# Optimization experiments

Measured on AMD Instinct MI355X. Metric: run time of the kernel, lower is better.

## Reference

```python
import jax, jax.numpy as jnp
import numpy as np

NUM_EXPERTS = 8
HIDDEN = 2048
INTER = 1408
N_TOKENS = 8192


def setup_inputs() -> dict:
    key = jax.random.key(0)
    k1, k2, k3, k4, k5 = jax.random.split(key, 5)
    tokens = jax.random.normal(k1, (N_TOKENS, HIDDEN), dtype=jnp.float32)
    local_ids = jax.random.randint(k2, (N_TOKENS,), 0, NUM_EXPERTS)
    weights = jax.random.uniform(k3, (N_TOKENS,), dtype=jnp.float32)
    # kaiming_uniform-ish init scale
    bound1 = 1.0 / np.sqrt(HIDDEN)
    bound2 = 1.0 / np.sqrt(INTER)
    gate_up_proj = jax.random.uniform(k4, (NUM_EXPERTS, 2 * INTER, HIDDEN), dtype=jnp.float32, minval=-bound1, maxval=bound1)
    down_proj = jax.random.uniform(k5, (NUM_EXPERTS, HIDDEN, INTER), dtype=jnp.float32, minval=-bound2, maxval=bound2)
    return {"tokens": tokens, "local_ids": local_ids, "weights": weights,
            "gate_up_proj": gate_up_proj, "down_proj": down_proj}


def reference(tokens, local_ids, weights, gate_up_proj, down_proj):
    # tokens: [N, D]; local_ids: [N]; weights: [N]
    # gate_up_proj: [E, 2I, D]; down_proj: [E, D, I]
    E = gate_up_proj.shape[0]
    out = jnp.zeros_like(tokens)
    for e in range(E):  # fixed small expert loop; masked dense GEMMs
        fc1 = tokens @ gate_up_proj[e].T              # [N, 2I]
        gate, up = jnp.split(fc1, 2, axis=-1)         # SwiGLU convention: first half is gate
        h = jax.nn.silu(gate) * up                    # fused SiLU*up
        h = h * weights[:, None]                      # routing weight before down_proj
        o = h @ down_proj[e].T                        # [N, D]
        out = out + jnp.where((local_ids == e)[:, None], o, 0.0)
    return out
```

## Files before the change

kernel.cpp:

```cpp
#include <hip/hip_runtime.h>
#include <stdint.h>

#define E_    8
#define D_    2048
#define I_    1408
#define TWOI_ 2816
#define N_    8192
#define BM    128
#define MAXTILES 72
#define MPAD  9216
#define MAXST 40
#define NCT1  11

typedef __bf16 bf16x8 __attribute__((ext_vector_type(8)));
typedef float  floatx4 __attribute__((ext_vector_type(4)));

#define M_CNT   0
#define M_CUR   8
#define M_PB    16
#define M_NT    24
#define M_RTE   32
#define M_RTR   104
#define M_RTV   176
#define M_NST   248
#define M_STE   256
#define M_STR   296
#define M_STV   336

#define OFF_PERM  4096ULL
#define OFF_WPAD  40960ULL
#define OFF_APAD  81920ULL
#define OFF_HPAD  37830656ULL
#define OFF_GU    63782912ULL
#define OFF_DN    156057600ULL
#define WS_NEED   202194944ULL

__device__ inline void gload16(const void* g, void* lds) {
  __builtin_amdgcn_global_load_lds(
      (__attribute__((address_space(1))) void*)g,
      (__attribute__((address_space(3))) void*)lds, 16, 0, 0);
}

__device__ inline unsigned short f2bf(float f) {
  unsigned int u = __builtin_bit_cast(unsigned int, f);
  u += 0x7fffu + ((u >> 16) & 1u);
  return (unsigned short)(u >> 16);
}

__global__ void k_hist(const int* __restrict__ ids, int* meta) {
  int i = blockIdx.x * 256 + threadIdx.x;
  int e = ids[i];
  int lane = threadIdx.x & 63;
  for (int ex = 0; ex < E_; ++ex) {
    unsigned long long m = __ballot(e == ex);
    if (lane == 0 && m) atomicAdd(&meta[M_CNT + ex], __popcll(m));
  }
}

__global__ void k_meta(int* meta) {
  if (threadIdx.x != 0) return;
  int padr = 0, tiles = 0;
  for (int e = 0; e < E_; ++e) {
    meta[M_PB + e] = padr;
    int c = meta[M_CNT + e];
    int nt = (c + BM - 1) / BM;
    for (int t = 0; t < nt; ++t) {
      meta[M_RTE + tiles] = e;
      meta[M_RTR + tiles] = padr + t * BM;
      int v = c - t * BM; if (v > BM) v = BM;
      meta[M_RTV + tiles] = v;
      tiles++;
    }
    padr += nt * BM;
  }
  meta[M_NT] = tiles;
  int nst = 0;
  for (int e = 0; e < E_; ++e) {
    int c = meta[M_CNT + e];
    int pb = meta[M_PB + e];
    for (int off = 0; off < c; off += 256) {
      meta[M_STE + nst] = e;
      meta[M_STR + nst] = pb + off;
      int v = c - off; if (v > 256) v = 256;
      meta[M_STV + nst] = v;
      nst++;
    }
  }
  meta[M_NST] = nst;
}

__global__ void k_scatter(const int* __restrict__ ids, const float* __restrict__ w,
                          int* meta, int* perm, float* wpad) {
  int i = blockIdx.x * 256 + threadIdx.x;
  int e = ids[i];
  float wv = w[i];
  int lane = threadIdx.x & 63;
  for (int ex = 0; ex < E_; ++ex) {
    unsigned long long m = __ballot(e == ex);
    if (!m) continue;
    int base = 0;
    if (lane == 0) base = atomicAdd(&meta[M_CUR + ex], __popcll(m));
    base = __shfl(base, 0);
    if (e == ex) {
      int r = meta[M_PB + ex] + base + __popcll(m & ((1ULL << lane) - 1ULL));
      perm[r] = i;
      wpad[r] = wv;
    }
  }
}

__global__ void k_gather(const float* __restrict__ tokens, const int* __restrict__ perm,
                         unsigned short* __restrict__ apad) {
  int r = blockIdx.x;
  int t = perm[r];
  if (t < 0) return;
  const float4* src = (const float4*)(tokens + (size_t)t * D_);
  uint4* dst = (uint4*)(apad + (size_t)r * D_);
  int i = threadIdx.x;
  float4 a = src[i * 2], b = src[i * 2 + 1];
  union { unsigned short s[8]; uint4 v; } pk;
  pk.s[0] = f2bf(a.x); pk.s[1] = f2bf(a.y); pk.s[2] = f2bf(a.z); pk.s[3] = f2bf(a.w);
  pk.s[4] = f2bf(b.x); pk.s[5] = f2bf(b.y); pk.s[6] = f2bf(b.z); pk.s[7] = f2bf(b.w);
  dst[i] = pk.v;
}

__global__ void k_cvt(const float* __restrict__ src, unsigned short* __restrict__ dst, int n8) {
  int i = blockIdx.x * 256 + threadIdx.x;
  if (i >= n8) return;
  const float4* s4 = (const float4*)src;
  float4 a = s4[i * 2], b = s4[i * 2 + 1];
  union { unsigned short s[8]; uint4 v; } pk;
  pk.s[0] = f2bf(a.x); pk.s[1] = f2bf(a.y); pk.s[2] = f2bf(a.z); pk.s[3] = f2bf(a.w);
  pk.s[4] = f2bf(b.x); pk.s[5] = f2bf(b.y); pk.s[6] = f2bf(b.z); pk.s[7] = f2bf(b.w);
  ((uint4*)dst)[i] = pk.v;
}


#define RD_A(h, s)                                                            \
  {                                                                           \
    const char* baseA_ = (const char*)&Abuf[s][h][0];                         \
    _Pragma("unroll") for (int mf = 0; mf < 4; ++mf) {                        \
      af[mf][0] = *(const bf16x8*)(baseA_ + rbA + mf * 2048 + swz0);          \
      af[mf][1] = *(const bf16x8*)(baseA_ + rbA + mf * 2048 + swz1);          \
    }                                                                         \
  }

#define RD_B(h, s)                                                            \
  {                                                                           \
    const char* baseB_ = (const char*)&Bbuf[s][h][0];                         \
    _Pragma("unroll") for (int nf = 0; nf < 2; ++nf) {                        \
      bq[nf][0] = *(const bf16x8*)(baseB_ + cbB + nf * 2048 + swz0);          \
      bq[nf][1] = *(const bf16x8*)(baseB_ + cbB + nf * 2048 + swz1);          \
    }                                                                         \
  }

#define MFMA_PH(qi)                                                           \
  __builtin_amdgcn_s_setprio(1);                                              \
  _Pragma("unroll") for (int mf = 0; mf < 4; ++mf) {                          \
    _Pragma("unroll") for (int nf = 0; nf < 2; ++nf) {                        \
      acc[qi][mf][nf] = __builtin_amdgcn_mfma_f32_16x16x32_bf16(              \
          af[mf][0], bq[nf][0], acc[qi][mf][nf], 0, 0, 0);                    \
      acc[qi][mf][nf] = __builtin_amdgcn_mfma_f32_16x16x32_bf16(              \
          af[mf][1], bq[nf][1], acc[qi][mf][nf], 0, 0, 0);                    \
    }                                                                         \
  }                                                                           \
  __builtin_amdgcn_s_setprio(0);

#define PH_MID()                                                              \
  __builtin_amdgcn_sched_barrier(0);                                          \
  __builtin_amdgcn_s_barrier();                                               \
  asm volatile("s_waitcnt lgkmcnt(0)" ::: "memory");                          \
  __builtin_amdgcn_sched_barrier(0);

#define PH_END()    __builtin_amdgcn_s_barrier();
#define PH_END_V6() asm volatile("s_waitcnt vmcnt(6)" ::: "memory"); \
                    __builtin_amdgcn_s_barrier();
#define PH_END_V8() asm volatile("s_waitcnt vmcnt(8)" ::: "memory"); \
                    __builtin_amdgcn_s_barrier();

#define STAGE(P, BUF, s, h)                                                   \
  gload16(P, &BUF[s][h][ldst]);                                               \
  gload16(P + 64 * D_, &BUF[s][h][4096 + ldst]);                              \
  P += 64;

__global__ __launch_bounds__(512, 2) void k_gemm1(
    const unsigned short* __restrict__ apad,
    const unsigned short* __restrict__ gub,
    const float* __restrict__ wpad,
    const int* __restrict__ meta,
    unsigned short* __restrict__ hpad) {
  int nst = meta[M_NST];
  int active = nst * NCT1;
  int bid = blockIdx.x;
  if (bid >= active) return;
  int x = bid & 7, idx = bid >> 3;
  int q = active >> 3, r = active & 7;
  int wgid = (x < r ? x * (q + 1) : r * (q + 1) + (x - r) * q) + idx;
  int st = wgid / NCT1;
  int ct = wgid - st * NCT1;
  int e = meta[M_STE + st], row0 = meta[M_STR + st], nv = meta[M_STV + st];

  __shared__ __attribute__((aligned(16))) __bf16 Abuf[2][2][128 * 64];
  __shared__ __attribute__((aligned(16))) __bf16 Bbuf[2][2][128 * 64];

  int tid = threadIdx.x;
  int lane = tid & 63;
  int wave = __builtin_amdgcn_readfirstlane(tid >> 6);
  int wm = wave >> 2, wn = wave & 3;
  int l16 = lane & 15, qd = lane >> 4;

  int r0 = tid >> 3;
  int jl8 = (((tid >> 3) ^ tid) & 7) * 8;
  const __bf16* pa0 = (const __bf16*)apad + (size_t)(row0 + r0) * D_ + jl8;
  const __bf16* pa1 = pa0 + (size_t)128 * D_;
  const __bf16* pb0 = (const __bf16*)gub +
      ((size_t)e * TWOI_ + (size_t)ct * 128 + r0) * D_ + jl8;
  const __bf16* pb1 = pb0 + (size_t)I_ * D_;
  int ldst = wave * 512;

  int swz0 = ((qd ^ (l16 & 7)) & 7) * 16;
  int swz1 = (((4 + qd) ^ (l16 & 7)) & 7) * 16;
  int rbA = (wm * 64 + l16) * 128;
  int cbB = (wn * 32 + l16) * 128;

  floatx4 zero = {0.f, 0.f, 0.f, 0.f};
  floatx4 acc[4][4][2];
#pragma unroll
  for (int a = 0; a < 4; ++a)
#pragma unroll
    for (int b = 0; b < 4; ++b)
#pragma unroll
      for (int c = 0; c < 2; ++c) acc[a][b][c] = zero;

  STAGE(pa0, Abuf, 0, 0)
  STAGE(pb0, Bbuf, 0, 0)
  STAGE(pa1, Abuf, 0, 1)
  STAGE(pb1, Bbuf, 0, 1)
  STAGE(pa0, Abuf, 1, 0)
  STAGE(pb0, Bbuf, 1, 0)
  asm volatile("s_waitcnt vmcnt(8)" ::: "memory");
  __builtin_amdgcn_s_barrier();

  bf16x8 af[4][2], bq[2][2];
  for (int t = 0; t < 32; t += 2) {
#pragma unroll
    for (int u = 0; u < 2; ++u) {
      int tl = t + u;
      RD_A(0, u)
      RD_B(0, u)
      if (tl + 1 < 32) { STAGE(pa1, Abuf, u ^ 1, 1) }
      PH_MID()
      MFMA_PH(0)
      PH_END_V6()
      RD_B(1, u)
      if (tl + 1 < 32) { STAGE(pb1, Bbuf, u ^ 1, 1) }
      PH_MID()
      MFMA_PH(1)
      PH_END()
      RD_A(1, u)
      RD_B(0, u)
      if (tl + 2 < 32) { STAGE(pa0, Abuf, u, 0) }
      PH_MID()
      MFMA_PH(2)
      PH_END()
      RD_B(1, u)
      if (tl + 2 < 32) { STAGE(pb0, Bbuf, u, 0) }
      PH_MID()
      MFMA_PH(3)
      PH_END_V8()
    }
  }

#pragma unroll
  for (int mi2 = 0; mi2 < 2; ++mi2)
#pragma unroll
    for (int mf = 0; mf < 4; ++mf)
#pragma unroll
      for (int reg = 0; reg < 4; ++reg) {
        int lr = mi2 * 128 + wm * 64 + mf * 16 + qd * 4 + reg;
        if (lr < nv) {
          float wgt = wpad[row0 + lr];
          unsigned short* hrow = hpad + (size_t)(row0 + lr) * I_ +
                                 (size_t)ct * 128 + wn * 32 + l16;
#pragma unroll
          for (int nf = 0; nf < 2; ++nf) {
            float g = acc[mi2 * 2 + 0][mf][nf][reg];
            float uu = acc[mi2 * 2 + 1][mf][nf][reg];
            float s = g / (1.f + __expf(-g));
            hrow[nf * 16] = f2bf(s * uu * wgt);
          }
        }
      }
}

__global__ __launch_bounds__(256) void k_gemm2(
    const unsigned short* __restrict__ hpad,
    const unsigned short* __restrict__ dnb,
    const int* __restrict__ meta,
    const int* __restrict__ perm,
    float* __restrict__ out) {
  int bid = blockIdx.x;
  int panel = bid / 128;
  int rem = bid - panel * 128;
  int ct = rem >> 3;
  int rt = panel * 8 + (rem & 7);
  if (rt >= meta[M_NT]) return;
  int e = meta[M_RTE + rt], row0 = meta[M_RTR + rt], nv = meta[M_RTV + rt];

  __shared__ __attribute__((aligned(16))) __bf16 As[2][128 * 32];
  __shared__ __attribute__((aligned(16))) __bf16 Bs[2][128 * 32];

  int tid = threadIdx.x;
  int lane = tid & 63;
  int wave = __builtin_amdgcn_readfirstlane(tid >> 6);
  int wm = wave >> 1, wn = wave & 1;

  const __bf16* A = (const __bf16*)hpad + (size_t)row0 * I_;
  const __bf16* B = (const __bf16*)dnb + ((size_t)e * D_ + (size_t)ct * 128) * I_;

  int srow = lane >> 2;
  int skq = (lane & 3) * 8;

  floatx4 zero = {0.f, 0.f, 0.f, 0.f};
  floatx4 acc[4][4];
#pragma unroll
  for (int mi = 0; mi < 4; ++mi)
#pragma unroll
    for (int ni = 0; ni < 4; ++ni) acc[mi][ni] = zero;

  int quad8 = (lane >> 4) * 8;
  int l16 = lane & 15;

  for (int k0 = 0; k0 < I_; k0 += 64) {
#pragma unroll
    for (int p = 0; p < 2; ++p) {
      int kk = k0 + p * 32;
      gload16(A + (size_t)(wave * 16 + srow) * I_ + kk + skq, &As[p][(wave * 16) * 32]);
      gload16(A + (size_t)(64 + wave * 16 + srow) * I_ + kk + skq, &As[p][(64 + wave * 16) * 32]);
      gload16(B + (size_t)(wave * 16 + srow) * I_ + kk + skq, &Bs[p][(wave * 16) * 32]);
      gload16(B + (size_t)(64 + wave * 16 + srow) * I_ + kk + skq, &Bs[p][(64 + wave * 16) * 32]);
    }
    __syncthreads();
#pragma unroll
    for (int p = 0; p < 2; ++p) {
      bf16x8 af[4], bfr[4];
#pragma unroll
      for (int mi = 0; mi < 4; ++mi)
        af[mi] = *(const bf16x8*)&As[p][(wm * 64 + mi * 16 + l16) * 32 + quad8];
#pragma unroll
      for (int ni = 0; ni < 4; ++ni)
        bfr[ni] = *(const bf16x8*)&Bs[p][(wn * 64 + ni * 16 + l16) * 32 + quad8];
#pragma unroll
      for (int mi = 0; mi < 4; ++mi)
#pragma unroll
        for (int ni = 0; ni < 4; ++ni)
          acc[mi][ni] = __builtin_amdgcn_mfma_f32_16x16x32_bf16(af[mi], bfr[ni], acc[mi][ni], 0, 0, 0);
    }
    __syncthreads();
  }

  int quad = lane >> 4;
#pragma unroll
  for (int mi = 0; mi < 4; ++mi)
#pragma unroll
    for (int reg = 0; reg < 4; ++reg) {
      int r = wm * 64 + mi * 16 + quad * 4 + reg;
      if (r < nv) {
        int t = perm[row0 + r];
        float* orow = out + (size_t)t * D_ + (size_t)ct * 128 + wn * 64;
#pragma unroll
        for (int ni = 0; ni < 4; ++ni)
          orow[ni * 16 + l16] = acc[mi][ni][reg];
      }
    }
}

__global__ __launch_bounds__(256) void k_naive(
    const float* __restrict__ tokens, const int* __restrict__ ids,
    const float* __restrict__ w, const float* __restrict__ gu,
    const float* __restrict__ dn, float* __restrict__ out) {
  __shared__ float tok[D_];
  __shared__ float h[I_];
  int t = blockIdx.x;
  int e = ids[t];
  float wgt = w[t];
  for (int i = threadIdx.x; i < D_; i += 256) tok[i] = tokens[(size_t)t * D_ + i];
  __syncthreads();
  for (int j = threadIdx.x; j < I_; j += 256) {
    const float* wg = gu + ((size_t)e * TWOI_ + j) * D_;
    const float* wu = wg + (size_t)I_ * D_;
    float g = 0.f, u = 0.f;
    for (int k = 0; k < D_; ++k) { g += tok[k] * wg[k]; u += tok[k] * wu[k]; }
    h[j] = g / (1.f + __expf(-g)) * u * wgt;
  }
  __syncthreads();
  for (int d = threadIdx.x; d < D_; d += 256) {
    const float* wd = dn + ((size_t)e * D_ + d) * I_;
    float acc = 0.f;
    for (int k = 0; k < I_; ++k) acc += h[k] * wd[k];
    out[(size_t)t * D_ + d] = acc;
  }
}

extern "C" void kernel_launch(void* const* d_in, const int* in_sizes, int n_in,
                              void* d_out, int out_size, void* d_ws, size_t ws_size,
                              hipStream_t stream) {
  const float* tokens = (const float*)d_in[0];
  const int*   ids    = (const int*)d_in[1];
  const float* wts    = (const float*)d_in[2];
  const float* gu     = (const float*)d_in[3];
  const float* dn     = (const float*)d_in[4];
  float* out = (float*)d_out;

  if (ws_size < (size_t)WS_NEED) {
    k_naive<<<N_, 256, 0, stream>>>(tokens, ids, wts, gu, dn, out);
    return;
  }

  char* ws = (char*)d_ws;
  int* meta = (int*)ws;
  int* perm = (int*)(ws + OFF_PERM);
  float* wpad = (float*)(ws + OFF_WPAD);
  unsigned short* apad = (unsigned short*)(ws + OFF_APAD);
  unsigned short* hpad = (unsigned short*)(ws + OFF_HPAD);
  unsigned short* gub  = (unsigned short*)(ws + OFF_GU);
  unsigned short* dnb  = (unsigned short*)(ws + OFF_DN);

  hipMemsetAsync(meta, 0, 64, stream);
  hipMemsetAsync(perm, 0xFF, MPAD * 4, stream);
  k_hist<<<N_ / 256, 256, 0, stream>>>(ids, meta);
  k_meta<<<1, 1, 0, stream>>>(meta);
  k_scatter<<<N_ / 256, 256, 0, stream>>>(ids, wts, meta, perm, wpad);
  k_gather<<<MPAD, 256, 0, stream>>>(tokens, perm, apad);
  int ngu8 = E_ * TWOI_ * D_ / 8;
  int ndn8 = E_ * D_ * I_ / 8;
  k_cvt<<<(ngu8 + 255) / 256, 256, 0, stream>>>(gu, gub, ngu8);
  k_cvt<<<(ndn8 + 255) / 256, 256, 0, stream>>>(dn, dnb, ndn8);
  k_gemm1<<<NCT1 * MAXST, 512, 0, stream>>>(apad, gub, wpad, meta, hpad);
  k_gemm2<<<9 * 128, 256, 0, stream>>>(hpad, dnb, meta, perm, out);
}
```

Baseline: 662.3 us.

## Restructure gemm1 main loop with two barriers per k-step and register-held gate/up B fragments

The k_gemm1 main loop is rewritten from four barrier-separated phases per k-step (each doing an LDS read, a global stage and an MFMA group) into one iteration with two barriers. Gate and up B fragments are kept in separate register sets so the A fragment can be reused across gate and up MFMAs. The next stage's LDS reads are prefetched during MFMA groups, and all four global loads for a stage are issued together. This cuts barrier and lgkmcnt wait overhead and improves overlap of LDS reads with MFMA, at the cost of more live registers and a tighter vmcnt ordering that is easy to get wrong.

```diff
diff --git a/kernel.cpp b/kernel.cpp
--- a/kernel.cpp
+++ b/kernel.cpp
@@ -136,52 +136,45 @@
 }
 
 
-#define RD_A(h, s)                                                            \
+#define RD_AF(h, s_)                                                          \
   {                                                                           \
-    const char* baseA_ = (const char*)&Abuf[s][h][0];                         \
+    const char* baseA_ = (const char*)&Abuf[s_][h][0];                        \
     _Pragma("unroll") for (int mf = 0; mf < 4; ++mf) {                        \
       af[mf][0] = *(const bf16x8*)(baseA_ + rbA + mf * 2048 + swz0);          \
       af[mf][1] = *(const bf16x8*)(baseA_ + rbA + mf * 2048 + swz1);          \
     }                                                                         \
   }
 
-#define RD_B(h, s)                                                            \
+#define RD_BX(bx, h, s_)                                                      \
   {                                                                           \
-    const char* baseB_ = (const char*)&Bbuf[s][h][0];                         \
+    const char* baseB_ = (const char*)&Bbuf[s_][h][0];                        \
     _Pragma("unroll") for (int nf = 0; nf < 2; ++nf) {                        \
-      bq[nf][0] = *(const bf16x8*)(baseB_ + cbB + nf * 2048 + swz0);          \
-      bq[nf][1] = *(const bf16x8*)(baseB_ + cbB + nf * 2048 + swz1);          \
+      bx[nf][0] = *(const bf16x8*)(baseB_ + cbB + nf * 2048 + swz0);          \
+      bx[nf][1] = *(const bf16x8*)(baseB_ + cbB + nf * 2048 + swz1);          \
     }                                                                         \
   }
 
-#define MFMA_PH(qi)                                                           \
-  __builtin_amdgcn_s_setprio(1);                                              \
+#define CL_PAIR(qi, bx)                                                       \
   _Pragma("unroll") for (int mf = 0; mf < 4; ++mf) {                          \
     _Pragma("unroll") for (int nf = 0; nf < 2; ++nf) {                        \
       acc[qi][mf][nf] = __builtin_amdgcn_mfma_f32_16x16x32_bf16(              \
-          af[mf][0], bq[nf][0], acc[qi][mf][nf], 0, 0, 0);                    \
+          af[mf][0], bx[nf][0], acc[qi][mf][nf], 0, 0, 0);                    \
       acc[qi][mf][nf] = __builtin_amdgcn_mfma_f32_16x16x32_bf16(              \
-          af[mf][1], bq[nf][1], acc[qi][mf][nf], 0, 0, 0);                    \
+          af[mf][1], bx[nf][1], acc[qi][mf][nf], 0, 0, 0);                    \
     }                                                                         \
-  }                                                                           \
-  __builtin_amdgcn_s_setprio(0);
-
-#define PH_MID()                                                              \
-  __builtin_amdgcn_sched_barrier(0);                                          \
-  __builtin_amdgcn_s_barrier();                                               \
-  asm volatile("s_waitcnt lgkmcnt(0)" ::: "memory");                          \
-  __builtin_amdgcn_sched_barrier(0);
-
-#define PH_END()    __builtin_amdgcn_s_barrier();
-#define PH_END_V6() asm volatile("s_waitcnt vmcnt(6)" ::: "memory"); \
-                    __builtin_amdgcn_s_barrier();
-#define PH_END_V8() asm volatile("s_waitcnt vmcnt(8)" ::: "memory"); \
-                    __builtin_amdgcn_s_barrier();
-
-#define STAGE(P, BUF, s, h)                                                   \
-  gload16(P, &BUF[s][h][ldst]);                                               \
-  gload16(P + 64 * D_, &BUF[s][h][4096 + ldst]);                              \
-  P += 64;
+  }
+
+#define STAGE4(s_)                                                            \
+  gload16(pa0, &Abuf[s_][0][ldst]);                                           \
+  gload16(pa0 + 64 * D_, &Abuf[s_][0][4096 + ldst]); pa0 += 64;               \
+  gload16(pb0, &Bbuf[s_][0][ldst]);                                           \
+  gload16(pb0 + 64 * D_, &Bbuf[s_][0][4096 + ldst]); pb0 += 64;               \
+  gload16(pb1, &Bbuf[s_][1][ldst]);                                           \
+  gload16(pb1 + 64 * D_, &Bbuf[s_][1][4096 + ldst]); pb1 += 64;               \
+  gload16(pa1, &Abuf[s_][1][ldst]);                                           \
+  gload16(pa1 + 64 * D_, &Abuf[s_][1][4096 + ldst]); pa1 += 64;
+
+#define SB0() __builtin_amdgcn_sched_barrier(0);
 
 __global__ __launch_bounds__(512, 2) void k_gemm1(
     const unsigned short* __restrict__ apad,
@@ -232,43 +225,45 @@
 #pragma unroll
       for (int c = 0; c < 2; ++c) acc[a][b][c] = zero;
 
-  STAGE(pa0, Abuf, 0, 0)
-  STAGE(pb0, Bbuf, 0, 0)
-  STAGE(pa1, Abuf, 0, 1)
-  STAGE(pb1, Bbuf, 0, 1)
-  STAGE(pa0, Abuf, 1, 0)
-  STAGE(pb0, Bbuf, 1, 0)
+  bf16x8 af[4][2], bg[2][2], bu[2][2];
+
+  STAGE4(0)
+  STAGE4(1)
   asm volatile("s_waitcnt vmcnt(8)" ::: "memory");
   __builtin_amdgcn_s_barrier();
-
-  bf16x8 af[4][2], bq[2][2];
-  for (int t = 0; t < 32; t += 2) {
-#pragma unroll
-    for (int u = 0; u < 2; ++u) {
-      int tl = t + u;
-      RD_A(0, u)
-      RD_B(0, u)
-      if (tl + 1 < 32) { STAGE(pa1, Abuf, u ^ 1, 1) }
-      PH_MID()
-      MFMA_PH(0)
-      PH_END_V6()
-      RD_B(1, u)
-      if (tl + 1 < 32) { STAGE(pb1, Bbuf, u ^ 1, 1) }
-      PH_MID()
-      MFMA_PH(1)
-      PH_END()
-      RD_A(1, u)
-      RD_B(0, u)
-      if (tl + 2 < 32) { STAGE(pa0, Abuf, u, 0) }
-      PH_MID()
-      MFMA_PH(2)
-      PH_END()
-      RD_B(1, u)
-      if (tl + 2 < 32) { STAGE(pb0, Bbuf, u, 0) }
-      PH_MID()
-      MFMA_PH(3)
-      PH_END_V8()
-    }
+  RD_BX(bu, 1, 0)
+  RD_BX(bg, 0, 0)
+  RD_AF(0, 0)
+
+  for (int t = 0; t < 32; ++t) {
+    int s = t & 1;
+    asm volatile("s_waitcnt lgkmcnt(0)" ::: "memory");
+    SB0()
+    __builtin_amdgcn_s_setprio(1);
+    CL_PAIR(0, bg)
+    CL_PAIR(1, bu)
+    __builtin_amdgcn_s_setprio(0);
+    RD_AF(1, s)
+    SB0()
+    asm volatile("s_waitcnt vmcnt(2)" ::: "memory");
+    asm volatile("s_waitcnt lgkmcnt(0)" ::: "memory");
+    SB0()
+    __builtin_amdgcn_s_barrier();
+    if (t < 30) { STAGE4(s) }
+    SB0()
+    __builtin_amdgcn_s_setprio(1);
+    CL_PAIR(3, bu)
+    __builtin_amdgcn_s_setprio(0);
+    if (t < 31) { RD_BX(bu, 1, s ^ 1) }
+    SB0()
+    __builtin_amdgcn_s_setprio(1);
+    CL_PAIR(2, bg)
+    __builtin_amdgcn_s_setprio(0);
+    if (t < 31) { RD_BX(bg, 0, s ^ 1) RD_AF(0, s ^ 1) }
+    SB0()
+    if (t < 30) { asm volatile("s_waitcnt vmcnt(8)" ::: "memory"); }
+    else        { asm volatile("s_waitcnt vmcnt(0)" ::: "memory"); }
+    __builtin_amdgcn_s_barrier();
   }
 
 #pragma unroll
@@ -286,8 +281,8 @@
           for (int nf = 0; nf < 2; ++nf) {
             float g = acc[mi2 * 2 + 0][mf][nf][reg];
             float uu = acc[mi2 * 2 + 1][mf][nf][reg];
-            float s = g / (1.f + __expf(-g));
-            hrow[nf * 16] = f2bf(s * uu * wgt);
+            float sg = g / (1.f + __expf(-g));
+            hrow[nf * 16] = f2bf(sg * uu * wgt);
           }
         }
       }
```

Measured after the change: 673.9 us. About the same (+1.7%).
